# Optimization experiments

Hardware: AMD Instinct MI355X
Metric: run time of the kernel (lower is better)

The kernel has to match this reference:

```python
import jax, jax.numpy as jnp
import numpy as np

G, S, L, F, D = 128, 2048, 256, 512, 512  # groups, sample_num, max_len, n_factor, attn dim


def setup_inputs() -> dict:
    key = jax.random.key(0)
    ks = jax.random.split(key, 16)
    s1, s2, s3, s4 = 1.0 / np.sqrt(D), 1.0 / np.sqrt(256), 1.0 / np.sqrt(128), 1.0 / np.sqrt(64)
    return {
        "raw": jax.random.normal(ks[0], (G, S, L), jnp.float32),        # padded input_1, item i -> raw[i,:,:n_i]
        "info": jax.random.normal(ks[1], (G, L, F), jnp.float32),       # padded input_2
        "Wq": jax.random.normal(ks[2], (F, D), jnp.float32) * 0.05,
        "Wk": jax.random.normal(ks[3], (F, D), jnp.float32) * 0.05,
        "Wv": jax.random.normal(ks[4], (F, D), jnp.float32) * 0.05,
        "W1": jax.random.normal(ks[5], (D, 256), jnp.float32) * s1,
        "b1": jax.random.normal(ks[6], (256,), jnp.float32) * s1,
        "W2": jax.random.normal(ks[7], (256, 128), jnp.float32) * s2,
        "b2": jax.random.normal(ks[8], (128,), jnp.float32) * s2,
        "W3": jax.random.normal(ks[9], (128, 64), jnp.float32) * s3,
        "b3": jax.random.normal(ks[10], (64,), jnp.float32) * s3,
        "W4": jax.random.normal(ks[11], (64, 1), jnp.float32) * s4,
        "b4": jax.random.normal(ks[12], (1,), jnp.float32) * s4,
        "lengths": jax.random.randint(ks[13], (G,), 1, L + 1),          # ragged lengths n_i in [1, L]
        "sample_num": S,
    }


def reference(raw, info, Wq, Wk, Wv, W1, b1, W2, b2, W3, b3, W4, b4, lengths, sample_num):
    Lmax = info.shape[1]
    key_mask = jnp.arange(Lmax)[None, :] < lengths[:, None]            # [G, L] valid positions
    # per-item self-attention (batched over items, masked over padding)
    Q = jnp.einsum('glf,fd->gld', info, Wq)
    K = jnp.einsum('glf,fd->gld', info, Wk)
    V = jnp.einsum('glf,fd->gld', info, Wv)
    scores = jnp.einsum('gld,gmd->glm', Q, K)
    scores = jnp.where(key_mask[:, None, :], scores, -jnp.inf)
    attn = jax.nn.softmax(scores, axis=-1)
    ctx = jnp.einsum('glm,gmd->gld', attn, V)                          # [G, L, D]
    # 4-layer linear scorer (no nonlinearity in the original)
    h = ctx @ W1 + b1
    h = h @ W2 + b2
    h = h @ W3 + b3
    w = (h @ W4 + b4)[..., 0]                                          # [G, L]
    # original: items with n_i == 1 get score_weight = ones(1,1)
    onehot0 = (jnp.arange(Lmax) == 0).astype(w.dtype)
    w = jnp.where((lengths == 1)[:, None], onehot0[None, :], w)
    w = w * key_mask.astype(w.dtype)                                   # zero padded positions
    # per-item raw @ weight, concatenated along dim 1 -> [sample_num, G]
    out = jnp.einsum('gsl,gl->sg', raw, w)
    return out
```

## Files before the change

kernel.cpp:

```cpp
#include <hip/hip_runtime.h>
#include <hip/hip_bf16.h>
#include <cstdint>
#include <cmath>

#define GG 128
#define SS 2048
#define LL 256
#define FF 512
#define DD 512

typedef __bf16 bf16_t;
typedef __bf16 bf16x8 __attribute__((ext_vector_type(8)));
typedef __bf16 bf16x4 __attribute__((ext_vector_type(4)));
typedef float  f32x4  __attribute__((ext_vector_type(4)));

#define MiB (1024UL * 1024UL)
#define OFF_INFO_HI (0 * MiB)
#define OFF_INFO_LO (32 * MiB)
#define OFF_T_HI    (64 * MiB)
#define OFF_T_LO    (96 * MiB)
#define OFF_S       (128 * MiB)
#define OFF_WQ_HI   (160 * MiB)
#define OFF_WQ_LO   (160 * MiB + 512 * 1024)
#define OFF_WK_HI   (161 * MiB)
#define OFF_WK_LO   (161 * MiB + 512 * 1024)
#define OFF_GT_HI   (162 * MiB)
#define OFF_GT_LO   (162 * MiB + 512 * 1024)
#define OFF_VEFF    (163 * MiB)
#define OFF_VW      (164 * MiB)
#define OFF_CC      (164 * MiB + 4096)
#define OFF_U       (164 * MiB + 8192)
#define OFF_V34     (164 * MiB + 12288)
#define OFF_T2      (164 * MiB + 12800)
#define OFF_V234    (164 * MiB + 13312)
#define OFF_T3      (164 * MiB + 14336)
#define OFF_WVEC    (165 * MiB)

__device__ __forceinline__ void gload16(const bf16_t* g, bf16_t* lds) {
  __builtin_amdgcn_global_load_lds(
      (const __attribute__((address_space(1))) void*)g,
      (__attribute__((address_space(3))) void*)lds, 16, 0, 0);
}

__global__ __launch_bounds__(256) void prep_fold1_kernel(
    const float* __restrict__ Wq, const float* __restrict__ Wk,
    const float* __restrict__ W3, const float* __restrict__ W4,
    const float* __restrict__ W2, const float* __restrict__ b1,
    const float* __restrict__ b2,
    bf16_t* __restrict__ Wq_hi, bf16_t* __restrict__ Wq_lo,
    bf16_t* __restrict__ Wk_hi, bf16_t* __restrict__ Wk_lo,
    float* __restrict__ v34, float* __restrict__ t2g) {
  const int b = blockIdx.x, t = threadIdx.x;
  if (b < 512) {
    const float* src = (b < 256) ? Wq : Wk;
    bf16_t* dhi = (b < 256) ? Wq_hi : Wk_hi;
    bf16_t* dlo = (b < 256) ? Wq_lo : Wk_lo;
    int i = (b & 255) * 256 + t;
    float4 v = *(const float4*)&src[(size_t)i * 4];
    float x[4] = {v.x, v.y, v.z, v.w};
    bf16x4 h, l;
#pragma unroll
    for (int e = 0; e < 4; ++e) {
      h[e] = (bf16_t)x[e];
      l[e] = (bf16_t)(x[e] - (float)h[e]);
    }
    *(bf16x4*)&dhi[(size_t)i * 4] = h;
    *(bf16x4*)&dlo[(size_t)i * 4] = l;
    return;
  }
  __shared__ float red[256];
  float acc = 0.f;
  if (b < 640) {
    const int row = b - 512;
    for (int k = t; k < 64; k += 256) acc += W3[row * 64 + k] * W4[k];
  } else {
    const int c = b - 640;
    for (int i = t; i < 256; i += 256) acc += b1[i] * W2[(size_t)i * 128 + c];
  }
  red[t] = acc;
  __syncthreads();
  if (t < 128) red[t] += red[t + 128];
  __syncthreads();
  if (t < 64) {
    float a = red[t] + red[t + 64];
#pragma unroll
    for (int off = 32; off > 0; off >>= 1) a += __shfl_down(a, off);
    if (t == 0) {
      if (b < 640) v34[b - 512] = a;
      else t2g[b - 640] = b2[b - 640] + a;
    }
  }
}

__global__ __launch_bounds__(256) void fold2_kernel(
    const float* __restrict__ M0, const float* __restrict__ v0,
    float* __restrict__ out0, int N0, int K0,
    const float* __restrict__ M1, const float* __restrict__ v1,
    const float* __restrict__ bias1, float* __restrict__ out1, int N1, int K1) {
  __shared__ float red[256];
  const int t = threadIdx.x;
  const int b = blockIdx.x;
  float acc = 0.f;
  if (b < N0) {
    const float* row = M0 + (size_t)b * K0;
    for (int k = t; k < K0; k += 256) acc += row[k] * v0[k];
  } else {
    const int c = b - N0;
    for (int i = t; i < K1; i += 256) acc += v1[i] * M1[(size_t)i * N1 + c];
  }
  red[t] = acc;
  __syncthreads();
  if (t < 128) red[t] += red[t + 128];
  __syncthreads();
  if (t < 64) {
    float a = red[t] + red[t + 64];
#pragma unroll
    for (int off = 32; off > 0; off >>= 1) a += __shfl_down(a, off);
    if (t == 0) {
      if (b < N0) out0[b] = a;
      else out1[b - N0] = bias1[b - N0] + a;
    }
  }
}

__global__ __launch_bounds__(256) void cast_veff_kernel(
    const float* __restrict__ info, const float* __restrict__ vweff,
    const int* __restrict__ lengths, bf16_t* __restrict__ hi,
    bf16_t* __restrict__ lo, float* __restrict__ veff) {
  __shared__ float vw[512];
  const int t = threadIdx.x, lane = t & 63, wv = t >> 6;
  vw[t] = vweff[t];
  vw[256 + t] = vweff[256 + t];
  __syncthreads();
  const int row = blockIdx.x * 4 + wv;
  const float* ip = info + (size_t)row * 512 + lane * 8;
  const float4 a = *(const float4*)ip;
  const float4 b = *(const float4*)(ip + 4);
  float x[8] = {a.x, a.y, a.z, a.w, b.x, b.y, b.z, b.w};
  bf16x8 h, l;
#pragma unroll
  for (int e = 0; e < 8; ++e) {
    h[e] = (bf16_t)x[e];
    l[e] = (bf16_t)(x[e] - (float)h[e]);
  }
  *(bf16x8*)&hi[(size_t)row * 512 + lane * 8] = h;
  *(bf16x8*)&lo[(size_t)row * 512 + lane * 8] = l;
  const int d0 = lane * 8;
  float acc = 0.f;
#pragma unroll
  for (int e = 0; e < 8; ++e) acc += x[e] * vw[d0 + e];
#pragma unroll
  for (int off = 32; off > 0; off >>= 1) acc += __shfl_down(acc, off);
  const int n = lengths[row >> 8];
  if (lane == 0) veff[row] = ((row & 255) < n) ? acc : 0.f;
}

template <int BN, bool ASPLIT, bool BSPLIT, int OUTMODE, int SKIP, bool SWIZ>
__global__ __launch_bounds__(256) void gemm_bt(
    const bf16_t* __restrict__ Ahi, const bf16_t* __restrict__ Alo, int lda, long sA,
    const bf16_t* __restrict__ Bhi, const bf16_t* __restrict__ Blo, int ldb, long sB,
    void* __restrict__ C0, void* __restrict__ C1, int ldc, long sC,
    int K, const int* __restrict__ lengths) {
  constexpr int BM = 128;
  constexpr int BK = 64;
  constexpr int WM = 4;
  constexpr int WN = BN / 32;
  constexpr int PA = BM * BK;
  constexpr int PB = BN * BK;
  constexpr int ITA = BM * 8 / 256;
  constexpr int ITB = BN * 8 / 256;
  __shared__ bf16_t As[(ASPLIT ? 2 : 1) * PA];
  __shared__ bf16_t Bs[(BSPLIT ? 2 : 1) * PB];

  const int gx = gridDim.x, gy = gridDim.y;
  int wgid = blockIdx.x + gx * (blockIdx.y + gy * blockIdx.z);
  if (SWIZ) {
    const int nwg = gx * gy * (int)gridDim.z;
    const int q = nwg >> 3;
    wgid = (wgid & 7) * q + (wgid >> 3);
  }
  const int xx = wgid % gx;
  const int rem = wgid / gx;
  const int yy = rem % gy;
  const int b = rem / gy;
  const int m0 = yy * BM;
  const int n0 = xx * BN;

  if (SKIP == 1) { if ((m0 & 255) >= lengths[m0 >> 8]) return; }
  if (SKIP == 3) { int n = lengths[b]; if (m0 >= n || n0 >= n) return; }

  const int t = threadIdx.x;
  const int lane = t & 63;
  const int wave = t >> 6;
  const int wm = (wave >> 1) * 64;
  const int wn = (wave & 1) * (BN / 2);

  const bf16_t* Ah = Ahi + (size_t)b * sA;
  const bf16_t* Al = ASPLIT ? Alo + (size_t)b * sA : nullptr;
  const bf16_t* Bh = Bhi + (size_t)b * sB;
  const bf16_t* Bl = BSPLIT ? Blo + (size_t)b * sB : nullptr;

  f32x4 acc[WM][WN];
#pragma unroll
  for (int i = 0; i < WM; ++i)
#pragma unroll
    for (int j = 0; j < WN; ++j) acc[i][j] = {0.f, 0.f, 0.f, 0.f};

  const int fr = lane & 15;
  const int fs = lane >> 4;
  const int sr = t >> 3, ssl = t & 7;

  for (int k0 = 0; k0 < K; k0 += BK) {
#pragma unroll
    for (int it = 0; it < ITA; ++it) {
      const int r = sr + it * 32;
      const size_t ga = (size_t)(m0 + r) * lda + k0 + ((ssl ^ (r & 7)) << 3);
      bf16_t* dst = &As[(it * 256 + wave * 64) * 8];
      gload16(&Ah[ga], dst);
      if (ASPLIT) gload16(&Al[ga], dst + PA);
    }
#pragma unroll
    for (int it = 0; it < ITB; ++it) {
      const int r = sr + it * 32;
      const size_t ga = (size_t)(n0 + r) * ldb + k0 + ((ssl ^ (r & 7)) << 3);
      bf16_t* dst = &Bs[(it * 256 + wave * 64) * 8];
      gload16(&Bh[ga], dst);
      if (BSPLIT) gload16(&Bl[ga], dst + PB);
    }
    asm volatile("s_waitcnt vmcnt(0)" ::: "memory");
    __builtin_amdgcn_sched_barrier(0);
    __syncthreads();
#pragma unroll
    for (int kk = 0; kk < 2; ++kk) {
      bf16x8 ah[WM], al[WM], bh[WN], bl[WN];
#pragma unroll
      for (int i = 0; i < WM; ++i) {
        int r = wm + i * 16 + fr;
        int la = r * BK + (((kk * 4 + fs) ^ (r & 7)) * 8);
        ah[i] = *(const bf16x8*)&As[la];
        if (ASPLIT) al[i] = *(const bf16x8*)&As[PA + la];
      }
#pragma unroll
      for (int j = 0; j < WN; ++j) {
        int r = wn + j * 16 + fr;
        int la = r * BK + (((kk * 4 + fs) ^ (r & 7)) * 8);
        bh[j] = *(const bf16x8*)&Bs[la];
        if (BSPLIT) bl[j] = *(const bf16x8*)&Bs[PB + la];
      }
#pragma unroll
      for (int i = 0; i < WM; ++i)
#pragma unroll
        for (int j = 0; j < WN; ++j) {
          acc[i][j] = __builtin_amdgcn_mfma_f32_16x16x32_bf16(ah[i], bh[j], acc[i][j], 0, 0, 0);
          if (BSPLIT)
            acc[i][j] = __builtin_amdgcn_mfma_f32_16x16x32_bf16(ah[i], bl[j], acc[i][j], 0, 0, 0);
          if (ASPLIT)
            acc[i][j] = __builtin_amdgcn_mfma_f32_16x16x32_bf16(al[i], bh[j], acc[i][j], 0, 0, 0);
        }
    }
    __syncthreads();
  }

#pragma unroll
  for (int i = 0; i < WM; ++i) {
#pragma unroll
    for (int j = 0; j < WN; ++j) {
      const int col = n0 + wn + j * 16 + fr;
#pragma unroll
      for (int jj = 0; jj < 4; ++jj) {
        const int row = m0 + wm + i * 16 + fs * 4 + jj;
        const float v = acc[i][j][jj];
        const size_t off = (size_t)b * sC + (size_t)row * ldc + col;
        if (OUTMODE == 0) {
          ((float*)C0)[off] = v;
        } else {
          bf16_t h = (bf16_t)v;
          ((bf16_t*)C0)[off] = h;
          ((bf16_t*)C1)[off] = (bf16_t)(v - (float)h);
        }
      }
    }
  }
}

__global__ __launch_bounds__(256) void softmax_dot_kernel(
    const float* __restrict__ S, const float* __restrict__ veff,
    const float* __restrict__ cc, const int* __restrict__ lengths,
    float* __restrict__ w) {
  const int t = threadIdx.x, lane = t & 63, wave = t >> 6;
  const int row = blockIdx.x * 4 + wave;
  const int g = row >> 8, l = row & 255;
  const int n = lengths[g];
  if (n == 1 || l >= n) {
    if (lane == 0) w[row] = (n == 1 && l == 0) ? 1.f : 0.f;
    return;
  }
  const float* srow = S + (size_t)row * 256;
  const int c0i = lane * 4;
  float4 v = *(const float4*)&srow[c0i];
  float4 vf = *(const float4*)&veff[g * 256 + c0i];
  float s[4] = {v.x, v.y, v.z, v.w};
  float ve[4] = {vf.x, vf.y, vf.z, vf.w};
  float m = -INFINITY;
#pragma unroll
  for (int e = 0; e < 4; ++e)
    if (c0i + e < n) m = fmaxf(m, s[e]);
#pragma unroll
  for (int off = 32; off > 0; off >>= 1) m = fmaxf(m, __shfl_xor(m, off));
  float sum = 0.f, dot = 0.f;
#pragma unroll
  for (int e = 0; e < 4; ++e) {
    if (c0i + e < n) {
      float ee = __expf(s[e] - m);
      sum += ee;
      dot += ee * ve[e];
    }
  }
#pragma unroll
  for (int off = 32; off > 0; off >>= 1) {
    sum += __shfl_xor(sum, off);
    dot += __shfl_xor(dot, off);
  }
  if (lane == 0) w[row] = dot / sum + cc[0];
}

__global__ __launch_bounds__(256) void out_kernel(
    const float* __restrict__ raw, const float* __restrict__ w,
    const int* __restrict__ lengths, float* __restrict__ out) {
  __shared__ float wl[LL];
  const int g = blockIdx.x;
  const int t = threadIdx.x;
  wl[t] = w[g * LL + t];
  __syncthreads();
  const int n = lengths[g];
  const int wave = t >> 6, lane = t & 63;
  const int s = blockIdx.y * 4 + wave;
  float acc = 0.f;
  if (lane * 4 < n) {
    const float4 r4 = *(const float4*)(raw + ((size_t)g * SS + s) * LL + lane * 4);
    const float4 w4v = *(const float4*)&wl[lane * 4];
    acc = r4.x * w4v.x + r4.y * w4v.y + r4.z * w4v.z + r4.w * w4v.w;
  }
#pragma unroll
  for (int off = 32; off > 0; off >>= 1) acc += __shfl_down(acc, off);
  if (lane == 0) out[(size_t)s * GG + g] = acc;
}

extern "C" void kernel_launch(void* const* d_in, const int* in_sizes, int n_in,
                              void* d_out, int out_size, void* d_ws, size_t ws_size,
                              hipStream_t stream) {
  const float* raw  = (const float*)d_in[0];
  const float* info = (const float*)d_in[1];
  const float* Wq   = (const float*)d_in[2];
  const float* Wk   = (const float*)d_in[3];
  const float* Wv   = (const float*)d_in[4];
  const float* W1   = (const float*)d_in[5];
  const float* b1   = (const float*)d_in[6];
  const float* W2   = (const float*)d_in[7];
  const float* b2   = (const float*)d_in[8];
  const float* W3   = (const float*)d_in[9];
  const float* b3   = (const float*)d_in[10];
  const float* W4   = (const float*)d_in[11];
  const float* b4   = (const float*)d_in[12];
  const int* lengths = (const int*)d_in[13];
  float* out = (float*)d_out;

  char* ws = (char*)d_ws;
  bf16_t* info_hi = (bf16_t*)(ws + OFF_INFO_HI);
  bf16_t* info_lo = (bf16_t*)(ws + OFF_INFO_LO);
  bf16_t* T_hi = (bf16_t*)(ws + OFF_T_HI);
  bf16_t* T_lo = (bf16_t*)(ws + OFF_T_LO);
  bf16_t* Wq_hi = (bf16_t*)(ws + OFF_WQ_HI);
  bf16_t* Wq_lo = (bf16_t*)(ws + OFF_WQ_LO);
  bf16_t* Wk_hi = (bf16_t*)(ws + OFF_WK_HI);
  bf16_t* Wk_lo = (bf16_t*)(ws + OFF_WK_LO);
  bf16_t* Gt_hi = (bf16_t*)(ws + OFF_GT_HI);
  bf16_t* Gt_lo = (bf16_t*)(ws + OFF_GT_LO);
  float*  S     = (float*)(ws + OFF_S);
  float*  veff  = (float*)(ws + OFF_VEFF);
  float*  vweff = (float*)(ws + OFF_VW);
  float*  cc    = (float*)(ws + OFF_CC);
  float*  u_g   = (float*)(ws + OFF_U);
  float*  v34   = (float*)(ws + OFF_V34);
  float*  t2g   = (float*)(ws + OFF_T2);
  float*  v234  = (float*)(ws + OFF_V234);
  float*  t3g   = (float*)(ws + OFF_T3);
  float*  w     = (float*)(ws + OFF_WVEC);

  dim3 blk(256);
  const int M = GG * LL;

  prep_fold1_kernel<<<dim3(768), blk, 0, stream>>>(
      Wq, Wk, W3, W4, W2, b1, b2, Wq_hi, Wq_lo, Wk_hi, Wk_lo, v34, t2g);

  fold2_kernel<<<dim3(320), blk, 0, stream>>>(
      W2, v34, v234, 256, 128, W3, t2g, b3, t3g, 64, 128);
  fold2_kernel<<<dim3(513), blk, 0, stream>>>(
      W1, v234, u_g, 512, 256, W4, t3g, b4, cc, 1, 64);
  fold2_kernel<<<dim3(512), blk, 0, stream>>>(
      Wv, u_g, vweff, 512, 512, W4, t3g, b4, cc, 0, 64);

  cast_veff_kernel<<<dim3(M / 4), blk, 0, stream>>>(info, vweff, lengths,
                                                    info_hi, info_lo, veff);

  gemm_bt<128, true, true, 2, 0, false><<<dim3(4, 4, 1), blk, 0, stream>>>(
      Wk_hi, Wk_lo, 512, 0, Wq_hi, Wq_lo, 512, 0, Gt_hi, Gt_lo, 512, 0, 512, nullptr);

  gemm_bt<128, true, true, 2, 1, true><<<dim3(4, M / 128, 1), blk, 0, stream>>>(
      info_hi, info_lo, 512, 0, Gt_hi, Gt_lo, 512, 0, T_hi, T_lo, 512, 0, 512, lengths);

  gemm_bt<128, true, true, 0, 3, true><<<dim3(2, 2, GG), blk, 0, stream>>>(
      T_hi, T_lo, 512, 256L * 512, info_hi, info_lo, 512, 256L * 512,
      S, nullptr, 256, 256L * 256, 512, lengths);

  softmax_dot_kernel<<<dim3(M / 4), blk, 0, stream>>>(S, veff, cc, lengths, w);

  out_kernel<<<dim3(GG, SS / 4), blk, 0, stream>>>(raw, w, lengths, out);
}
```

Before: 200.8 us.

## Double-buffer LDS in split-bf16 GEMM and skip padded rows in cast kernel

```diff
diff --git a/kernel.cpp b/kernel.cpp
--- a/kernel.cpp
+++ b/kernel.cpp
@@ -133,6 +133,14 @@
   vw[256 + t] = vweff[256 + t];
   __syncthreads();
   const int row = blockIdx.x * 4 + wv;
+  const int n = lengths[row >> 8];
+  if ((row & 255) >= n) {
+    bf16x8 z = {};
+    *(bf16x8*)&hi[(size_t)row * 512 + lane * 8] = z;
+    *(bf16x8*)&lo[(size_t)row * 512 + lane * 8] = z;
+    if (lane == 0) veff[row] = 0.f;
+    return;
+  }
   const float* ip = info + (size_t)row * 512 + lane * 8;
   const float4 a = *(const float4*)ip;
   const float4 b = *(const float4*)(ip + 4);
@@ -151,26 +159,23 @@
   for (int e = 0; e < 8; ++e) acc += x[e] * vw[d0 + e];
 #pragma unroll
   for (int off = 32; off > 0; off >>= 1) acc += __shfl_down(acc, off);
-  const int n = lengths[row >> 8];
-  if (lane == 0) veff[row] = ((row & 255) < n) ? acc : 0.f;
-}
-
-template <int BN, bool ASPLIT, bool BSPLIT, int OUTMODE, int SKIP, bool SWIZ>
-__global__ __launch_bounds__(256) void gemm_bt(
+  if (lane == 0) veff[row] = acc;
+}
+
+template <int BN, int OUTMODE, int SKIP, bool SWIZ>
+__global__ __launch_bounds__(256) void gemm_bt2(
     const bf16_t* __restrict__ Ahi, const bf16_t* __restrict__ Alo, int lda, long sA,
     const bf16_t* __restrict__ Bhi, const bf16_t* __restrict__ Blo, int ldb, long sB,
     void* __restrict__ C0, void* __restrict__ C1, int ldc, long sC,
     int K, const int* __restrict__ lengths) {
   constexpr int BM = 128;
-  constexpr int BK = 64;
+  constexpr int BK = 32;
   constexpr int WM = 4;
   constexpr int WN = BN / 32;
   constexpr int PA = BM * BK;
   constexpr int PB = BN * BK;
-  constexpr int ITA = BM * 8 / 256;
-  constexpr int ITB = BN * 8 / 256;
-  __shared__ bf16_t As[(ASPLIT ? 2 : 1) * PA];
-  __shared__ bf16_t Bs[(BSPLIT ? 2 : 1) * PB];
+  __shared__ bf16_t As[2][2][PA];
+  __shared__ bf16_t Bs[2][2][PB];
 
   const int gx = gridDim.x, gy = gridDim.y;
   int wgid = blockIdx.x + gx * (blockIdx.y + gy * blockIdx.z);
@@ -196,9 +201,9 @@
   const int wn = (wave & 1) * (BN / 2);
 
   const bf16_t* Ah = Ahi + (size_t)b * sA;
-  const bf16_t* Al = ASPLIT ? Alo + (size_t)b * sA : nullptr;
+  const bf16_t* Al = Alo + (size_t)b * sA;
   const bf16_t* Bh = Bhi + (size_t)b * sB;
-  const bf16_t* Bl = BSPLIT ? Blo + (size_t)b * sB : nullptr;
+  const bf16_t* Bl = Blo + (size_t)b * sB;
 
   f32x4 acc[WM][WN];
 #pragma unroll
@@ -208,56 +213,80 @@
 
   const int fr = lane & 15;
   const int fs = lane >> 4;
-  const int sr = t >> 3, ssl = t & 7;
-
-  for (int k0 = 0; k0 < K; k0 += BK) {
-#pragma unroll
-    for (int it = 0; it < ITA; ++it) {
-      const int r = sr + it * 32;
-      const size_t ga = (size_t)(m0 + r) * lda + k0 + ((ssl ^ (r & 7)) << 3);
-      bf16_t* dst = &As[(it * 256 + wave * 64) * 8];
+  const int sr = t >> 2, ssl = t & 3;
+
+  const int nsteps = K / BK;
+
+  {
+#pragma unroll
+    for (int it = 0; it < BM / 64; ++it) {
+      const int r = sr + it * 64;
+      const size_t ga = (size_t)(m0 + r) * lda + ((ssl ^ ((r >> 1) & 3)) << 3);
+      bf16_t* dst = &As[0][0][(it * 256 + wave * 64) * 8];
       gload16(&Ah[ga], dst);
-      if (ASPLIT) gload16(&Al[ga], dst + PA);
-    }
-#pragma unroll
-    for (int it = 0; it < ITB; ++it) {
-      const int r = sr + it * 32;
-      const size_t ga = (size_t)(n0 + r) * ldb + k0 + ((ssl ^ (r & 7)) << 3);
-      bf16_t* dst = &Bs[(it * 256 + wave * 64) * 8];
+      gload16(&Al[ga], dst + PA);
+    }
+#pragma unroll
+    for (int it = 0; it < BN / 64; ++it) {
+      const int r = sr + it * 64;
+      const size_t ga = (size_t)(n0 + r) * ldb + ((ssl ^ ((r >> 1) & 3)) << 3);
+      bf16_t* dst = &Bs[0][0][(it * 256 + wave * 64) * 8];
       gload16(&Bh[ga], dst);
-      if (BSPLIT) gload16(&Bl[ga], dst + PB);
-    }
+      gload16(&Bl[ga], dst + PB);
+    }
+  }
+  asm volatile("s_waitcnt vmcnt(0)" ::: "memory");
+  __builtin_amdgcn_sched_barrier(0);
+  __syncthreads();
+
+#pragma unroll 2
+  for (int s = 0; s < nsteps; ++s) {
+    const int cur = s & 1;
+    if (s + 1 < nsteps) {
+      const int k0 = (s + 1) * BK;
+      const int nxt = (s + 1) & 1;
+#pragma unroll
+      for (int it = 0; it < BM / 64; ++it) {
+        const int r = sr + it * 64;
+        const size_t ga = (size_t)(m0 + r) * lda + k0 + ((ssl ^ ((r >> 1) & 3)) << 3);
+        bf16_t* dst = &As[nxt][0][(it * 256 + wave * 64) * 8];
+        gload16(&Ah[ga], dst);
+        gload16(&Al[ga], dst + PA);
+      }
+#pragma unroll
+      for (int it = 0; it < BN / 64; ++it) {
+        const int r = sr + it * 64;
+        const size_t ga = (size_t)(n0 + r) * ldb + k0 + ((ssl ^ ((r >> 1) & 3)) << 3);
+        bf16_t* dst = &Bs[nxt][0][(it * 256 + wave * 64) * 8];
+        gload16(&Bh[ga], dst);
+        gload16(&Bl[ga], dst + PB);
+      }
+    }
+    bf16x8 ah[WM], al[WM], bh[WN], bl[WN];
+#pragma unroll
+    for (int i = 0; i < WM; ++i) {
+      int r = wm + i * 16 + fr;
+      int la = r * BK + ((fs ^ ((r >> 1) & 3)) * 8);
+      ah[i] = *(const bf16x8*)&As[cur][0][la];
+      al[i] = *(const bf16x8*)&As[cur][1][la];
+    }
+#pragma unroll
+    for (int j = 0; j < WN; ++j) {
+      int r = wn + j * 16 + fr;
+      int la = r * BK + ((fs ^ ((r >> 1) & 3)) * 8);
+      bh[j] = *(const bf16x8*)&Bs[cur][0][la];
+      bl[j] = *(const bf16x8*)&Bs[cur][1][la];
+    }
+#pragma unroll
+    for (int i = 0; i < WM; ++i)
+#pragma unroll
+      for (int j = 0; j < WN; ++j) {
+        acc[i][j] = __builtin_amdgcn_mfma_f32_16x16x32_bf16(ah[i], bh[j], acc[i][j], 0, 0, 0);
+        acc[i][j] = __builtin_amdgcn_mfma_f32_16x16x32_bf16(ah[i], bl[j], acc[i][j], 0, 0, 0);
+        acc[i][j] = __builtin_amdgcn_mfma_f32_16x16x32_bf16(al[i], bh[j], acc[i][j], 0, 0, 0);
+      }
     asm volatile("s_waitcnt vmcnt(0)" ::: "memory");
     __builtin_amdgcn_sched_barrier(0);
-    __syncthreads();
-#pragma unroll
-    for (int kk = 0; kk < 2; ++kk) {
-      bf16x8 ah[WM], al[WM], bh[WN], bl[WN];
-#pragma unroll
-      for (int i = 0; i < WM; ++i) {
-        int r = wm + i * 16 + fr;
-        int la = r * BK + (((kk * 4 + fs) ^ (r & 7)) * 8);
-        ah[i] = *(const bf16x8*)&As[la];
-        if (ASPLIT) al[i] = *(const bf16x8*)&As[PA + la];
-      }
-#pragma unroll
-      for (int j = 0; j < WN; ++j) {
-        int r = wn + j * 16 + fr;
-        int la = r * BK + (((kk * 4 + fs) ^ (r & 7)) * 8);
-        bh[j] = *(const bf16x8*)&Bs[la];
-        if (BSPLIT) bl[j] = *(const bf16x8*)&Bs[PB + la];
-      }
-#pragma unroll
-      for (int i = 0; i < WM; ++i)
-#pragma unroll
-        for (int j = 0; j < WN; ++j) {
-          acc[i][j] = __builtin_amdgcn_mfma_f32_16x16x32_bf16(ah[i], bh[j], acc[i][j], 0, 0, 0);
-          if (BSPLIT)
-            acc[i][j] = __builtin_amdgcn_mfma_f32_16x16x32_bf16(ah[i], bl[j], acc[i][j], 0, 0, 0);
-          if (ASPLIT)
-            acc[i][j] = __builtin_amdgcn_mfma_f32_16x16x32_bf16(al[i], bh[j], acc[i][j], 0, 0, 0);
-        }
-    }
     __syncthreads();
   }
 
@@ -403,13 +432,13 @@
   cast_veff_kernel<<<dim3(M / 4), blk, 0, stream>>>(info, vweff, lengths,
                                                     info_hi, info_lo, veff);
 
-  gemm_bt<128, true, true, 2, 0, false><<<dim3(4, 4, 1), blk, 0, stream>>>(
+  gemm_bt2<128, 2, 0, false><<<dim3(4, 4, 1), blk, 0, stream>>>(
       Wk_hi, Wk_lo, 512, 0, Wq_hi, Wq_lo, 512, 0, Gt_hi, Gt_lo, 512, 0, 512, nullptr);
 
-  gemm_bt<128, true, true, 2, 1, true><<<dim3(4, M / 128, 1), blk, 0, stream>>>(
+  gemm_bt2<128, 2, 1, true><<<dim3(4, M / 128, 1), blk, 0, stream>>>(
       info_hi, info_lo, 512, 0, Gt_hi, Gt_lo, 512, 0, T_hi, T_lo, 512, 0, 512, lengths);
 
-  gemm_bt<128, true, true, 0, 3, true><<<dim3(2, 2, GG), blk, 0, stream>>>(
+  gemm_bt2<128, 0, 3, true><<<dim3(2, 2, GG), blk, 0, stream>>>(
       T_hi, T_lo, 512, 256L * 512, info_hi, info_lo, 512, 256L * 512,
       S, nullptr, 256, 256L * 256, 512, lengths);
 
```

Measured after the change: 209.0 us. 4.1% more time.
